# Kernel optimization log

Hardware: AMD Instinct MI355X
Metric: run time of the kernel (lower is better)

The kernel has to match this reference:

```python
import jax, jax.numpy as jnp
import numpy as np

NUM_LABELS = 64  # number of distinct label ids (0 = background, unchanged)


def setup_inputs() -> dict:
    key = jax.random.key(0)
    k1, k2, k3 = jax.random.split(key, 3)
    shape = (2, 192, 256, 256)
    texturized = jax.random.normal(k1, shape, dtype=jnp.float32)
    label_map = jax.random.randint(k2, shape, 0, NUM_LABELS, dtype=jnp.int32)
    # one Uniform(0, intensity) draw per label, mirroring self.intensity() per loop iter
    intensities = jax.random.uniform(k3, (NUM_LABELS,), dtype=jnp.float32)
    return {"texturized": texturized, "label_map": label_map, "intensities": intensities}


def reference(texturized, label_map, intensities):
    # Per label l > 0 (torch loop): adjusted[mask_l] -= mean(tex[mask_l] - intensity_l)
    #                             = tex - (segment_mean_l - intensity_l) on mask_l.
    flat_tex = texturized.reshape(-1)
    flat_lab = label_map.reshape(-1)
    sums = jax.ops.segment_sum(flat_tex, flat_lab, num_segments=NUM_LABELS)
    counts = jax.ops.segment_sum(jnp.ones_like(flat_tex), flat_lab, num_segments=NUM_LABELS)
    means = sums / jnp.maximum(counts, 1.0)
    delta = means - intensities  # [NUM_LABELS] per-label bls.mean()
    adj = flat_tex - jnp.where(flat_lab > 0, delta[flat_lab], 0.0)
    return adj.reshape(texturized.shape)
```

## Files before the change

### kernel.cpp

```cpp
#include <hip/hip_runtime.h>
#include <stdint.h>

#define NL 64
#define RBLOCKS 2560

typedef float f32x4 __attribute__((ext_vector_type(4)));

__global__ __launch_bounds__(64) void tl_reduce(const float* __restrict__ tex,
                                                const int* __restrict__ lab,
                                                float* __restrict__ part,
                                                int n) {
    __shared__ unsigned int s_bin[NL * 64];
    const int tid = threadIdx.x;

#pragma unroll
    for (int j = 0; j < NL; ++j) s_bin[(j << 6) | tid] = 0u;
    __syncthreads();

    const int n4 = n >> 2;
    const float4* __restrict__ tex4 = (const float4*)tex;
    const int4* __restrict__ lab4 = (const int4*)lab;
    const int stride = RBLOCKS * 64;

#define UPD(t, l)                                                            \
    {                                                                        \
        s_bin[(((l).x & (NL - 1)) << 6) | tid] +=                            \
            (1u << 26) + (unsigned int)fmaf((t).x, 32768.0f, 524288.5f);     \
        s_bin[(((l).y & (NL - 1)) << 6) | tid] +=                            \
            (1u << 26) + (unsigned int)fmaf((t).y, 32768.0f, 524288.5f);     \
        s_bin[(((l).z & (NL - 1)) << 6) | tid] +=                            \
            (1u << 26) + (unsigned int)fmaf((t).z, 32768.0f, 524288.5f);     \
        s_bin[(((l).w & (NL - 1)) << 6) | tid] +=                            \
            (1u << 26) + (unsigned int)fmaf((t).w, 32768.0f, 524288.5f);     \
    }

    int iA = blockIdx.x * 64 + tid;
    if (iA < n4) {
        float4 tA = tex4[iA];
        int4 lA = lab4[iA];
        int iB = iA + stride;
        for (;;) {
            const bool vB = iB < n4;
            float4 tB;
            int4 lB;
            if (vB) { tB = tex4[iB]; lB = lab4[iB]; }
            UPD(tA, lA);
            if (!vB) break;
            const int iC = iB + stride;
            const bool vC = iC < n4;
            if (vC) { tA = tex4[iC]; lA = lab4[iC]; }
            UPD(tB, lB);
            if (!vC) break;
            iB = iC + stride;
        }
    }

    if (blockIdx.x == 0) {
        const int base = n4 << 2;
        if (tid < n - base) {
            const int j = base + tid;
            s_bin[((lab[j] & (NL - 1)) << 6) | tid] +=
                (1u << 26) + (unsigned int)fmaf(tex[j], 32768.0f, 524288.5f);
        }
    }
    __syncthreads();

    {
        unsigned int cnt = 0u;
        double fx = 0.0;
#pragma unroll
        for (int j = 0; j < 64; ++j) {
            const unsigned int w = s_bin[(tid << 6) | ((j + tid) & 63)];
            cnt += w >> 26;
            fx += (double)(w & 0x03FFFFFFu);
        }
        const double s = fx * (1.0 / 32768.0) - 16.0 * (double)cnt;
        part[tid * RBLOCKS + blockIdx.x] = (float)s;
        part[(NL + tid) * RBLOCKS + blockIdx.x] = (float)cnt;
    }
}

__global__ __launch_bounds__(256) void tl_mid(const float* __restrict__ part,
                                              float* __restrict__ g_sums,
                                              float* __restrict__ g_cnts) {
    const int l = blockIdx.x;
    const int tid = threadIdx.x;
    double s = 0.0, c = 0.0;
    for (int b = tid; b < RBLOCKS; b += 256) {
        s += part[l * RBLOCKS + b];
        c += part[(NL + l) * RBLOCKS + b];
    }
    for (int off = 32; off; off >>= 1) {
        s += __shfl_down(s, off);
        c += __shfl_down(c, off);
    }
    __shared__ double sh[2][4];
    const int w = tid >> 6;
    if ((tid & 63) == 0) { sh[0][w] = s; sh[1][w] = c; }
    __syncthreads();
    if (tid == 0) {
        g_sums[l] = (float)(sh[0][0] + sh[0][1] + sh[0][2] + sh[0][3]);
        g_cnts[l] = (float)(sh[1][0] + sh[1][1] + sh[1][2] + sh[1][3]);
    }
}

__global__ __launch_bounds__(256) void tl_apply(const float* __restrict__ tex,
                                                const int* __restrict__ lab,
                                                const float* __restrict__ g_sums,
                                                const float* __restrict__ g_cnts,
                                                const float* __restrict__ intens,
                                                float* __restrict__ out, int n) {
    __shared__ float s_delta[NL];
    if (threadIdx.x < NL) {
        const int l = threadIdx.x;
        const float mean = g_sums[l] / fmaxf(g_cnts[l], 1.0f);
        s_delta[l] = (l > 0) ? (mean - intens[l]) : 0.0f;
    }
    __syncthreads();

    const int n4 = n >> 2;
    const int i = blockIdx.x * 256 + threadIdx.x;
    if (i < n4) {
        const float4 t = ((const float4*)tex)[i];
        const int4 l = ((const int4*)lab)[i];
        float4 o;
        o.x = t.x - s_delta[l.x & (NL - 1)];
        o.y = t.y - s_delta[l.y & (NL - 1)];
        o.z = t.z - s_delta[l.z & (NL - 1)];
        o.w = t.w - s_delta[l.w & (NL - 1)];
        __builtin_nontemporal_store(*(const f32x4*)&o, (f32x4*)&((float4*)out)[i]);
    }
    if (blockIdx.x == 0) {
        const int base = n4 << 2;
        if ((int)threadIdx.x < n - base) {
            const int j = base + threadIdx.x;
            out[j] = tex[j] - s_delta[lab[j] & (NL - 1)];
        }
    }
}

extern "C" void kernel_launch(void* const* d_in, const int* in_sizes, int n_in,
                              void* d_out, int out_size, void* d_ws, size_t ws_size,
                              hipStream_t stream) {
    const float* tex    = (const float*)d_in[0];
    const int*   lab    = (const int*)d_in[1];
    const float* intens = (const float*)d_in[2];
    float* out = (float*)d_out;
    const int n = in_sizes[0];

    float* part   = (float*)d_out;
    float* g_sums = (float*)d_ws;
    float* g_cnts = (float*)((char*)d_ws + NL * sizeof(float));

    tl_reduce<<<RBLOCKS, 64, 0, stream>>>(tex, lab, part, n);
    tl_mid<<<NL, 256, 0, stream>>>(part, g_sums, g_cnts);

    const int n4 = n >> 2;
    const int ablocks = (n4 + 255) / 256;
    tl_apply<<<ablocks, 256, 0, stream>>>(tex, lab, g_sums, g_cnts, intens, out, n);
}
```

Before: 292.0 us.

## Widen histogram blocks, merge duplicate labels per vector, grid-stride apply kernel

The reduction kernel now runs 128 threads per block over half as many blocks, with a private per-thread bin column in 32 KB of shared memory. Each thread combines equal-label lanes of its float4 in registers before doing the read-modify-write, which removes LDS dependency hazards between the four updates. The final per-label fold now uses two threads per label joined by a shuffle, and there are half as many partials for tl_mid to read. The apply kernel becomes a grid-stride loop over 4096 blocks that processes two float4s per iteration for more memory-level parallelism. The costs are extra compare and select work per element and lower occupancy from the larger shared-memory footprint.

```diff
diff --git a/kernel.cpp b/kernel.cpp
--- a/kernel.cpp
+++ b/kernel.cpp
@@ -2,39 +2,52 @@
 #include <stdint.h>
 
 #define NL 64
-#define RBLOCKS 2560
+#define RB 1280
+#define BT 128
 
 typedef float f32x4 __attribute__((ext_vector_type(4)));
 
-__global__ __launch_bounds__(64) void tl_reduce(const float* __restrict__ tex,
+#define FP(x) ((1u << 26) + (unsigned int)fmaf((x), 32768.0f, 524288.5f))
+
+static __device__ __forceinline__ void upd(unsigned int* __restrict__ s_bin,
+                                           int tid, float4 t, int4 l) {
+    const int a0 = ((l.x & (NL - 1)) << 7) | tid;
+    const int a1 = ((l.y & (NL - 1)) << 7) | tid;
+    const int a2 = ((l.z & (NL - 1)) << 7) | tid;
+    const int a3 = ((l.w & (NL - 1)) << 7) | tid;
+    unsigned int v0 = FP(t.x), v1 = FP(t.y), v2 = FP(t.z), v3 = FP(t.w);
+    const bool e10 = (a1 == a0);
+    const bool e20 = (a2 == a0), e21 = (a2 == a1);
+    const bool e30 = (a3 == a0), e31 = (a3 == a1), e32 = (a3 == a2);
+    v0 += (e10 ? v1 : 0u) + (e20 ? v2 : 0u) + (e30 ? v3 : 0u);
+    v1 += (e21 ? v2 : 0u) + (e31 ? v3 : 0u);
+    v2 += (e32 ? v3 : 0u);
+    const unsigned int t0 = s_bin[a0];
+    const unsigned int t1 = s_bin[a1];
+    const unsigned int t2 = s_bin[a2];
+    const unsigned int t3 = s_bin[a3];
+    s_bin[a0] = t0 + v0;
+    if (!e10) s_bin[a1] = t1 + v1;
+    if (!(e20 | e21)) s_bin[a2] = t2 + v2;
+    if (!(e30 | e31 | e32)) s_bin[a3] = t3 + v3;
+}
+
+__global__ __launch_bounds__(BT) void tl_reduce(const float* __restrict__ tex,
                                                 const int* __restrict__ lab,
                                                 float* __restrict__ part,
                                                 int n) {
-    __shared__ unsigned int s_bin[NL * 64];
+    __shared__ unsigned int s_bin[NL * BT];
     const int tid = threadIdx.x;
 
-#pragma unroll
-    for (int j = 0; j < NL; ++j) s_bin[(j << 6) | tid] = 0u;
+    for (int j = tid; j < NL * BT; j += BT) s_bin[j] = 0u;
     __syncthreads();
 
     const int n4 = n >> 2;
     const float4* __restrict__ tex4 = (const float4*)tex;
     const int4* __restrict__ lab4 = (const int4*)lab;
-    const int stride = RBLOCKS * 64;
-
-#define UPD(t, l)                                                            \
-    {                                                                        \
-        s_bin[(((l).x & (NL - 1)) << 6) | tid] +=                            \
-            (1u << 26) + (unsigned int)fmaf((t).x, 32768.0f, 524288.5f);     \
-        s_bin[(((l).y & (NL - 1)) << 6) | tid] +=                            \
-            (1u << 26) + (unsigned int)fmaf((t).y, 32768.0f, 524288.5f);     \
-        s_bin[(((l).z & (NL - 1)) << 6) | tid] +=                            \
-            (1u << 26) + (unsigned int)fmaf((t).z, 32768.0f, 524288.5f);     \
-        s_bin[(((l).w & (NL - 1)) << 6) | tid] +=                            \
-            (1u << 26) + (unsigned int)fmaf((t).w, 32768.0f, 524288.5f);     \
-    }
-
-    int iA = blockIdx.x * 64 + tid;
+    const int stride = RB * BT;
+
+    int iA = blockIdx.x * BT + tid;
     if (iA < n4) {
         float4 tA = tex4[iA];
         int4 lA = lab4[iA];
@@ -44,12 +57,12 @@
             float4 tB;
             int4 lB;
             if (vB) { tB = tex4[iB]; lB = lab4[iB]; }
-            UPD(tA, lA);
+            upd(s_bin, tid, tA, lA);
             if (!vB) break;
             const int iC = iB + stride;
             const bool vC = iC < n4;
             if (vC) { tA = tex4[iC]; lA = lab4[iC]; }
-            UPD(tB, lB);
+            upd(s_bin, tid, tB, lB);
             if (!vC) break;
             iB = iC + stride;
         }
@@ -59,24 +72,30 @@
         const int base = n4 << 2;
         if (tid < n - base) {
             const int j = base + tid;
-            s_bin[((lab[j] & (NL - 1)) << 6) | tid] +=
-                (1u << 26) + (unsigned int)fmaf(tex[j], 32768.0f, 524288.5f);
+            s_bin[((lab[j] & (NL - 1)) << 7) | tid] += FP(tex[j]);
         }
     }
     __syncthreads();
 
     {
+        const int label = tid >> 1;
+        const int half = tid & 1;
         unsigned int cnt = 0u;
         double fx = 0.0;
 #pragma unroll
         for (int j = 0; j < 64; ++j) {
-            const unsigned int w = s_bin[(tid << 6) | ((j + tid) & 63)];
+            const unsigned int w =
+                s_bin[(label << 7) | (half << 6) | ((j + tid) & 63)];
             cnt += w >> 26;
             fx += (double)(w & 0x03FFFFFFu);
         }
-        const double s = fx * (1.0 / 32768.0) - 16.0 * (double)cnt;
-        part[tid * RBLOCKS + blockIdx.x] = (float)s;
-        part[(NL + tid) * RBLOCKS + blockIdx.x] = (float)cnt;
+        cnt += __shfl_xor(cnt, 1);
+        fx += __shfl_xor(fx, 1);
+        if (half == 0) {
+            const double s = fx * (1.0 / 32768.0) - 16.0 * (double)cnt;
+            part[label * RB + blockIdx.x] = (float)s;
+            part[(NL + label) * RB + blockIdx.x] = (float)cnt;
+        }
     }
 }
 
@@ -86,9 +105,9 @@
     const int l = blockIdx.x;
     const int tid = threadIdx.x;
     double s = 0.0, c = 0.0;
-    for (int b = tid; b < RBLOCKS; b += 256) {
-        s += part[l * RBLOCKS + b];
-        c += part[(NL + l) * RBLOCKS + b];
+    for (int b = tid; b < RB; b += 256) {
+        s += part[l * RB + b];
+        c += part[(NL + l) * RB + b];
     }
     for (int off = 32; off; off >>= 1) {
         s += __shfl_down(s, off);
@@ -118,22 +137,45 @@
     }
     __syncthreads();
 
+    const int tid = threadIdx.x;
     const int n4 = n >> 2;
-    const int i = blockIdx.x * 256 + threadIdx.x;
-    if (i < n4) {
-        const float4 t = ((const float4*)tex)[i];
-        const int4 l = ((const int4*)lab)[i];
+    const float4* __restrict__ tex4 = (const float4*)tex;
+    const int4* __restrict__ lab4 = (const int4*)lab;
+    float4* __restrict__ out4 = (float4*)out;
+    const int st = gridDim.x * 256;
+
+    int i = blockIdx.x * 256 + tid;
+    while (i < n4) {
+        const int i2 = i + st;
+        const bool v2 = i2 < n4;
+        const float4 tA = tex4[i];
+        const int4 lA = lab4[i];
+        float4 tB;
+        int4 lB;
+        if (v2) { tB = tex4[i2]; lB = lab4[i2]; }
+
         float4 o;
-        o.x = t.x - s_delta[l.x & (NL - 1)];
-        o.y = t.y - s_delta[l.y & (NL - 1)];
-        o.z = t.z - s_delta[l.z & (NL - 1)];
-        o.w = t.w - s_delta[l.w & (NL - 1)];
-        __builtin_nontemporal_store(*(const f32x4*)&o, (f32x4*)&((float4*)out)[i]);
-    }
+        o.x = tA.x - s_delta[lA.x & (NL - 1)];
+        o.y = tA.y - s_delta[lA.y & (NL - 1)];
+        o.z = tA.z - s_delta[lA.z & (NL - 1)];
+        o.w = tA.w - s_delta[lA.w & (NL - 1)];
+        __builtin_nontemporal_store(*(const f32x4*)&o, (f32x4*)&out4[i]);
+
+        if (v2) {
+            float4 p;
+            p.x = tB.x - s_delta[lB.x & (NL - 1)];
+            p.y = tB.y - s_delta[lB.y & (NL - 1)];
+            p.z = tB.z - s_delta[lB.z & (NL - 1)];
+            p.w = tB.w - s_delta[lB.w & (NL - 1)];
+            __builtin_nontemporal_store(*(const f32x4*)&p, (f32x4*)&out4[i2]);
+        }
+        i = i2 + st;
+    }
+
     if (blockIdx.x == 0) {
         const int base = n4 << 2;
-        if ((int)threadIdx.x < n - base) {
-            const int j = base + threadIdx.x;
+        if (tid < n - base) {
+            const int j = base + tid;
             out[j] = tex[j] - s_delta[lab[j] & (NL - 1)];
         }
     }
@@ -152,10 +194,7 @@
     float* g_sums = (float*)d_ws;
     float* g_cnts = (float*)((char*)d_ws + NL * sizeof(float));
 
-    tl_reduce<<<RBLOCKS, 64, 0, stream>>>(tex, lab, part, n);
+    tl_reduce<<<RB, BT, 0, stream>>>(tex, lab, part, n);
     tl_mid<<<NL, 256, 0, stream>>>(part, g_sums, g_cnts);
-
-    const int n4 = n >> 2;
-    const int ablocks = (n4 + 255) / 256;
-    tl_apply<<<ablocks, 256, 0, stream>>>(tex, lab, g_sums, g_cnts, intens, out, n);
-}
+    tl_apply<<<4096, 256, 0, stream>>>(tex, lab, g_sums, g_cnts, intens, out, n);
+}
```

Measured after the change: 289.3 us. About the same (-0.9%).
